# Kernel tuning notes

Hardware: AMD Instinct MI355X
Metric: run time of the kernel (lower is better)

Reference implementation:

```python
import jax, jax.numpy as jnp
import numpy as np

B, C_IN, IMG, P, G, E, H = 4, 3, 576, 16, 36, 768, 12
T = G * G  # 1296 tokens
HD = E // H  # 64
LN_EPS = 1e-5


def layer_norm(x, g, b):
    mu = jnp.mean(x, axis=-1, keepdims=True)
    var = jnp.mean((x - mu) ** 2, axis=-1, keepdims=True)
    return (x - mu) * jax.lax.rsqrt(var + LN_EPS) * g + b


def setup_inputs() -> dict:
    key = jax.random.key(0)
    ks = jax.random.split(key, 12)
    s = lambda *sh: 0.02
    return {
        "x": jax.random.normal(ks[0], (B, C_IN, IMG, IMG), jnp.float32),
        "conv_w": jax.random.normal(ks[1], (E, C_IN, P, P), jnp.float32) * 0.02,
        "conv_b": jnp.zeros((E,), jnp.float32),
        "wq": jax.random.normal(ks[2], (E, E), jnp.float32) * 0.02,
        "wk": jax.random.normal(ks[3], (E, E), jnp.float32) * 0.02,
        "wv": jax.random.normal(ks[4], (E, E), jnp.float32) * 0.02,
        "wo": jax.random.normal(ks[5], (E, E), jnp.float32) * 0.02,
        "bo": jnp.zeros((E,), jnp.float32),
        "w1": jax.random.normal(ks[6], (E, 4 * E), jnp.float32) * 0.02,
        "b1": jnp.zeros((4 * E,), jnp.float32),
        "w2": jax.random.normal(ks[7], (4 * E, E), jnp.float32) * 0.02,
        "b2": jnp.zeros((E,), jnp.float32),
        "ln1_g": jnp.ones((E,), jnp.float32),
        "ln1_b": jnp.zeros((E,), jnp.float32),
        "ln2_g": jnp.ones((E,), jnp.float32),
        "ln2_b": jnp.zeros((E,), jnp.float32),
    }


def reference(x, conv_w, conv_b, wq, wk, wv, wo, bo, w1, b1, w2, b2,
              ln1_g, ln1_b, ln2_g, ln2_b):
    # --- patch embed: stride==kernel conv as patch reshape + einsum ---
    xr = x.reshape(B, C_IN, G, P, G, P)  # b c i p j q
    tok = jnp.einsum('bcipjq,ecpq->bije', xr, conv_w) + conv_b
    tok = tok.reshape(B, T, E)  # row-major (i,j) matches flatten(2).transpose

    # --- causal multi-head attention (scale uses n_embd, as in source) ---
    h = layer_norm(tok, ln1_g, ln1_b)
    q = (h @ wq).reshape(B, T, H, HD)
    k = (h @ wk).reshape(B, T, H, HD)
    v = (h @ wv).reshape(B, T, H, HD)
    scores = jnp.einsum('bqhd,bkhd->bhqk', q, k) * (E ** -0.5)
    mask = jnp.tril(jnp.ones((T, T), bool))
    scores = jnp.where(mask, scores, -jnp.inf)
    attn = jax.nn.softmax(scores, axis=-1)
    ao = jnp.einsum('bhqk,bkhd->bqhd', attn, v).reshape(B, T, E)
    tok = tok + (ao @ wo + bo)

    # --- MLP ---
    h2 = layer_norm(tok, ln2_g, ln2_b)
    tok = tok + (jax.nn.relu(h2 @ w1 + b1) @ w2 + b2)

    # --- back to image grid ---
    return tok.reshape(B, G, G, E).transpose(0, 3, 1, 2)
```

## Files before the change

kernel.cpp:

```cpp
#include <hip/hip_runtime.h>

typedef unsigned short u16;
typedef unsigned int u32;
typedef unsigned long long u64;
typedef float f32x4 __attribute__((ext_vector_type(4)));
typedef __bf16 bf16x8 __attribute__((ext_vector_type(8)));
typedef u16 u16x8 __attribute__((ext_vector_type(8)));

#define DEV __device__ __forceinline__


DEV u16 f2bf(float f) {
    union { float f; u32 u; } un; un.f = f;
    u32 u = un.u;
    return (u16)((u + 0x7fffu + ((u >> 16) & 1u)) >> 16);
}

DEV void gll16(const u16* src, u16* dst) {
    auto g = (const __attribute__((address_space(1))) u32*)(src);
    auto s = (__attribute__((address_space(3))) u32*)(dst);
    __builtin_amdgcn_global_load_lds(g, s, 16, 0, 0);
}

__global__ void convcvt_k(const float* __restrict__ src, u16* __restrict__ dst) {
    int i = blockIdx.x * 256 + threadIdx.x;
    f32x4 v = ((const f32x4*)src)[i];
    union { u16 q[4]; u64 ll; } un;
    #pragma unroll
    for (int j = 0; j < 4; ++j) un.q[j] = f2bf(v[j]);
    ((u64*)dst)[i] = un.ll;
}

__global__ void wtrans_k(const float* __restrict__ src, u16* __restrict__ dst, int K, int N) {
    __shared__ float tile[32][33];
    int n0 = blockIdx.x * 32, k0 = blockIdx.y * 32;
    int tx = threadIdx.x & 31, ty = threadIdx.x >> 5;
    #pragma unroll
    for (int i = 0; i < 32; i += 8)
        tile[ty + i][tx] = src[(size_t)(k0 + ty + i) * N + n0 + tx];
    __syncthreads();
    #pragma unroll
    for (int i = 0; i < 32; i += 8)
        dst[(size_t)(n0 + ty + i) * K + k0 + tx] = f2bf(tile[tx][ty + i]);
}

__global__ void patch_k(const float* __restrict__ x, u16* __restrict__ out) {
    int idx = blockIdx.x * 256 + threadIdx.x;
    int j = idx % 36; int r1 = idx / 36;
    int p = r1 % 16;  int r2 = r1 / 16;
    int i = r2 % 36;  int r3 = r2 / 36;
    int c = r3 % 3;   int b = r3 / 3;
    const f32x4* src = (const f32x4*)(x + (size_t)((b * 3 + c) * 576 + i * 16 + p) * 576 + j * 16);
    u16x8 lo, hi;
    #pragma unroll
    for (int k = 0; k < 2; ++k) {
        f32x4 v = src[k];
        #pragma unroll
        for (int e = 0; e < 4; ++e) lo[k * 4 + e] = f2bf(v[e]);
    }
    #pragma unroll
    for (int k = 0; k < 2; ++k) {
        f32x4 v = src[2 + k];
        #pragma unroll
        for (int e = 0; e < 4; ++e) hi[k * 4 + e] = f2bf(v[e]);
    }
    u16* dst = out + (size_t)(b * 1296 + i * 36 + j) * 768 + c * 256 + p * 16;
    *(u16x8*)dst = lo;
    *(u16x8*)(dst + 8) = hi;
}

__global__ __launch_bounds__(256) void ln_k(const float* __restrict__ x, const float* __restrict__ g,
                                            const float* __restrict__ bta, u16* __restrict__ out) {
    int row = blockIdx.x * 4 + (threadIdx.x >> 6);
    int l = threadIdx.x & 63;
    const float* xr = x + (size_t)row * 768;
    float v[12]; float s = 0.f, s2 = 0.f;
    #pragma unroll
    for (int i = 0; i < 12; ++i) { v[i] = xr[l + 64 * i]; s += v[i]; s2 += v[i] * v[i]; }
    #pragma unroll
    for (int off = 32; off; off >>= 1) { s += __shfl_xor(s, off); s2 += __shfl_xor(s2, off); }
    float mu = s * (1.f / 768.f);
    float var = s2 * (1.f / 768.f) - mu * mu;
    float rs = rsqrtf(var + 1e-5f);
    u16* orow = out + (size_t)row * 768;
    #pragma unroll
    for (int i = 0; i < 12; ++i) {
        int c = l + 64 * i;
        orow[c] = f2bf((v[i] - mu) * rs * g[c] + bta[c]);
    }
}

__global__ void vtrans_k(const u16* __restrict__ qkv, u16* __restrict__ vt) {
    __shared__ u16 tile[32][33];
    int bh = blockIdx.z; int b = bh / 12, h = bh % 12;
    int t0 = blockIdx.x * 32, d0 = blockIdx.y * 32;
    int tx = threadIdx.x & 31, ty = threadIdx.x >> 5;
    #pragma unroll
    for (int i = 0; i < 32; i += 8) {
        int t = t0 + ty + i; int tc = min(t, 1295);
        tile[ty + i][tx] = qkv[(size_t)(b * 1296 + tc) * 2304 + 1536 + h * 64 + d0 + tx];
    }
    __syncthreads();
    #pragma unroll
    for (int i = 0; i < 32; i += 8) {
        int d = d0 + ty + i; int t = t0 + tx;
        if (t < 1296) vt[(size_t)(bh * 64 + d) * 1344 + t] = tile[tx][ty + i];
    }
}

template <int BN, int EPI>
__global__ __launch_bounds__(256) void gemm_k(const u16* __restrict__ A, const u16* __restrict__ Bt,
                                              const float* __restrict__ bias, const float* __restrict__ resid,
                                              void* __restrict__ Cout, int K, int ldc, int nbx) {
    constexpr int M = 5184;
    constexpr int NF = BN / 32;
    __shared__ __align__(16) u16 lds[2][(128 + BN) * 64];
    const int tid = threadIdx.x;
    const int l = tid & 63, w = tid >> 6;
    const int lr = l & 15, lq = l >> 4;
    const int wm = w >> 1, wn = w & 1;

    const int total = nbx * 41;
    const int q = total >> 3, r = total & 7;
    const int x = blockIdx.x & 7;
    const int j = blockIdx.x >> 3;
    const int wrk = x * q + min(x, r) + j;
    const int by = wrk / nbx, bx = wrk - by * nbx;
    const int bm = by * 128;
    const int bn = bx * BN;

    f32x4 acc[4][NF];
    f32x4 zz = {0.f, 0.f, 0.f, 0.f};
    #pragma unroll
    for (int i = 0; i < 4; ++i)
        #pragma unroll
        for (int jj = 0; jj < NF; ++jj) acc[i][jj] = zz;

    const int nk = K >> 6;

    auto stage = [&](int buf, int kt) {
        u16* abase = &lds[buf][0];
        #pragma unroll
        for (int i = 0; i < 4; ++i) {
            int slot = tid + i * 256;
            int row = slot >> 3, piece = slot & 7;
            int sp = piece ^ (row & 7);
            const u16* src = A + (size_t)min(bm + row, M - 1) * K + kt * 64 + sp * 8;
            gll16(src, abase + ((tid & ~63) + i * 256) * 8);
        }
        u16* bbase = &lds[buf][128 * 64];
        #pragma unroll
        for (int i = 0; i < NF; ++i) {
            int slot = tid + i * 256;
            int row = slot >> 3, piece = slot & 7;
            int sp = piece ^ (row & 7);
            const u16* src = Bt + (size_t)(bn + row) * K + kt * 64 + sp * 8;
            gll16(src, bbase + ((tid & ~63) + i * 256) * 8);
        }
    };

    stage(0, 0);
    __syncthreads();
    for (int kt = 0; kt < nk; ++kt) {
        int cur = kt & 1;
        if (kt + 1 < nk) stage(cur ^ 1, kt + 1);
        bf16x8 af[4][2], bfr[NF][2];
        #pragma unroll
        for (int mi = 0; mi < 4; ++mi) {
            int row = wm * 64 + mi * 16 + lr;
            #pragma unroll
            for (int ks = 0; ks < 2; ++ks)
                af[mi][ks] = *(const bf16x8*)&lds[cur][row * 64 + (((lq + 4 * ks) ^ (row & 7)) << 3)];
        }
        #pragma unroll
        for (int ni = 0; ni < NF; ++ni) {
            int row = wn * (BN / 2) + ni * 16 + lr;
            #pragma unroll
            for (int ks = 0; ks < 2; ++ks)
                bfr[ni][ks] = *(const bf16x8*)&lds[cur][128 * 64 + row * 64 + (((lq + 4 * ks) ^ (row & 7)) << 3)];
        }
        #pragma unroll
        for (int mi = 0; mi < 4; ++mi)
            #pragma unroll
            for (int ni = 0; ni < NF; ++ni) {
                acc[mi][ni] = __builtin_amdgcn_mfma_f32_16x16x32_bf16(af[mi][0], bfr[ni][0], acc[mi][ni], 0, 0, 0);
                acc[mi][ni] = __builtin_amdgcn_mfma_f32_16x16x32_bf16(af[mi][1], bfr[ni][1], acc[mi][ni], 0, 0, 0);
            }
        __syncthreads();
    }

    #pragma unroll
    for (int mi = 0; mi < 4; ++mi) {
        #pragma unroll
        for (int ni = 0; ni < NF; ++ni) {
            int col = bn + wn * (BN / 2) + ni * 16 + lr;
            float bv = 0.f;
            if constexpr (EPI != 1) bv = bias[col];
            #pragma unroll
            for (int rr = 0; rr < 4; ++rr) {
                int m = bm + wm * 64 + mi * 16 + 4 * lq + rr;
                if (m < M) {
                    float v = acc[mi][ni][rr] + bv;
                    if constexpr (EPI == 2) v = fmaxf(v, 0.f);
                    if constexpr (EPI == 3 || EPI == 4) v += resid[(size_t)m * ldc + col];
                    if constexpr (EPI == 0 || EPI == 3) {
                        ((float*)Cout)[(size_t)m * ldc + col] = v;
                    } else if constexpr (EPI == 4) {
                        int b = m / 1296, t = m - b * 1296;
                        ((float*)Cout)[(size_t)(b * 768 + col) * 1296 + t] = v;
                    } else {
                        ((u16*)Cout)[(size_t)m * ldc + col] = f2bf(v);
                    }
                }
            }
        }
    }
}

__global__ __launch_bounds__(256, 2) void attn_k(const u16* __restrict__ qkv, const u16* __restrict__ vt,
                                                 u16* __restrict__ ao) {
    const float SCALE = 0.03608439182435161f;
    __shared__ __align__(16) u16 kv[2][2][4096];
    __shared__ __align__(16) u16 plds[4][16 * 72];
    const int tid = threadIdx.x;
    const int wid = tid >> 6, l = tid & 63;
    const int id = blockIdx.x;
    const int xr = id & 7, sl = id >> 3;
    const int g = sl / 11, bx = sl - g * 11;
    const int bh = g * 8 + xr;
    const int b = bh / 12, h = bh % 12;
    const int uu = bx * 4 + wid;
    const int u = min(uu, 40);
    const bool valid = (uu <= 40);
    const int lr = l & 15, lq = l >> 4;
    const int q0S = 16 * u, q0L = 16 * (80 - u);
    const bool hasS = valid && (u < 40);
    const int nktS = (u < 40) ? (((q0S + 15) >> 6) + 1) : 0;
    const int nktL = ((q0L + 15) >> 6) + 1;
    const int umin = min(bx * 4, 40);
    const int nktmax = ((16 * (80 - umin) + 15) >> 6) + 1;

    const u16* kbase = qkv + (size_t)(b * 1296) * 2304 + 768 + h * 64;
    const u16* vbase = vt + (size_t)bh * 64 * 1344;
    u16* pl = &plds[wid][0];

    const u16* qpS = qkv + (size_t)(b * 1296 + q0S + lr) * 2304 + h * 64;
    const u16* qpL = qkv + (size_t)(b * 1296 + q0L + lr) * 2304 + h * 64;
    bf16x8 qS0 = *(const bf16x8*)(qpS + 8 * lq);
    bf16x8 qS1 = *(const bf16x8*)(qpS + 32 + 8 * lq);
    bf16x8 qL0 = *(const bf16x8*)(qpL + 8 * lq);
    bf16x8 qL1 = *(const bf16x8*)(qpL + 32 + 8 * lq);

    f32x4 zz = {0.f, 0.f, 0.f, 0.f};
    f32x4 oS[4], oL[4];
    float mS[4], mL[4], lSs[4], lLs[4];
    #pragma unroll
    for (int i = 0; i < 4; ++i) {
        oS[i] = zz; oL[i] = zz;
        mS[i] = -__builtin_inff(); mL[i] = -__builtin_inff();
        lSs[i] = 0.f; lLs[i] = 0.f;
    }

    auto stage = [&](int buf, int kt) {
        const int k0 = kt * 64;
        #pragma unroll
        for (int i = 0; i < 2; ++i) {
            int slot = tid + i * 256;
            int row = slot >> 3;
            int piece = slot & 7;
            int sp = piece ^ (row & 7);
            int tc = min(k0 + row, 1295);
            gll16(kbase + (size_t)tc * 2304 + sp * 8,
                  &kv[buf][0][((tid & 0xFFFFFFC0) + i * 256) * 8]);
        }
        #pragma unroll
        for (int i = 0; i < 2; ++i) {
            int slot = tid + i * 256;
            int row = slot >> 3;
            int piece = slot & 7;
            int sp = piece ^ (row & 7);
            gll16(vbase + (size_t)row * 1344 + k0 + sp * 8,
                  &kv[buf][1][((tid & 0xFFFFFFC0) + i * 256) * 8]);
        }
    };

    bf16x8 kb[4][2], vb[4][2];

    auto visit = [&](int q0, bf16x8 qa0, bf16x8 qa1, f32x4 (&o)[4],
                     float (&mrow)[4], float (&lsum)[4], int k0) {
        f32x4 s[4];
        #pragma unroll
        for (int nt = 0; nt < 4; ++nt) {
            f32x4 a = zz;
            a = __builtin_amdgcn_mfma_f32_16x16x32_bf16(qa0, kb[nt][0], a, 0, 0, 0);
            a = __builtin_amdgcn_mfma_f32_16x16x32_bf16(qa1, kb[nt][1], a, 0, 0, 0);
            s[nt] = a;
        }
        float tmax[4];
        #pragma unroll
        for (int r = 0; r < 4; ++r) {
            int qrow = q0 + 4 * lq + r;
            #pragma unroll
            for (int nt = 0; nt < 4; ++nt) {
                int tcol = k0 + nt * 16 + lr;
                float val = s[nt][r] * SCALE;
                s[nt][r] = (tcol <= qrow) ? val : -__builtin_inff();
            }
            tmax[r] = fmaxf(fmaxf(s[0][r], s[1][r]), fmaxf(s[2][r], s[3][r]));
        }
        #pragma unroll
        for (int off = 1; off < 16; off <<= 1)
            #pragma unroll
            for (int r = 0; r < 4; ++r) tmax[r] = fmaxf(tmax[r], __shfl_xor(tmax[r], off));
        float alpha[4], tsum[4];
        #pragma unroll
        for (int r = 0; r < 4; ++r) {
            float nm = fmaxf(mrow[r], tmax[r]);
            alpha[r] = __expf(mrow[r] - nm);
            mrow[r] = nm;
            float accp = 0.f;
            #pragma unroll
            for (int nt = 0; nt < 4; ++nt) {
                float p = __expf(s[nt][r] - nm);
                s[nt][r] = p;
                accp += p;
            }
            tsum[r] = accp;
        }
        #pragma unroll
        for (int off = 1; off < 16; off <<= 1)
            #pragma unroll
            for (int r = 0; r < 4; ++r) tsum[r] += __shfl_xor(tsum[r], off);
        #pragma unroll
        for (int r = 0; r < 4; ++r) lsum[r] = lsum[r] * alpha[r] + tsum[r];
        #pragma unroll
        for (int dt = 0; dt < 4; ++dt)
            #pragma unroll
            for (int r = 0; r < 4; ++r) o[dt][r] *= alpha[r];
        #pragma unroll
        for (int nt = 0; nt < 4; ++nt)
            #pragma unroll
            for (int r = 0; r < 4; ++r)
                pl[(4 * lq + r) * 72 + nt * 16 + lr] = f2bf(s[nt][r]);
        __builtin_amdgcn_wave_barrier();
        bf16x8 pa0 = *(const bf16x8*)&pl[lr * 72 + 8 * lq];
        bf16x8 pa1 = *(const bf16x8*)&pl[lr * 72 + 32 + 8 * lq];
        #pragma unroll
        for (int dt = 0; dt < 4; ++dt) {
            o[dt] = __builtin_amdgcn_mfma_f32_16x16x32_bf16(pa0, vb[dt][0], o[dt], 0, 0, 0);
            o[dt] = __builtin_amdgcn_mfma_f32_16x16x32_bf16(pa1, vb[dt][1], o[dt], 0, 0, 0);
        }
        __builtin_amdgcn_wave_barrier();
    };

    stage(0, 0);
    for (int kt = 0; kt < nktmax; ++kt) {
        const int cur = kt & 1;
        const int k0 = kt * 64;
        __syncthreads();
        if (kt + 1 < nktmax) stage(cur ^ 1, kt + 1);
        #pragma unroll
        for (int nt = 0; nt < 4; ++nt) {
            int krow = nt * 16 + lr;
            kb[nt][0] = *(const bf16x8*)&kv[cur][0][krow * 64 + ((lq ^ (krow & 7)) << 3)];
            kb[nt][1] = *(const bf16x8*)&kv[cur][0][krow * 64 + (((lq + 4) ^ (krow & 7)) << 3)];
        }
        #pragma unroll
        for (int dt = 0; dt < 4; ++dt) {
            int vrow = dt * 16 + lr;
            vb[dt][0] = *(const bf16x8*)&kv[cur][1][vrow * 64 + ((lq ^ (vrow & 7)) << 3)];
            vb[dt][1] = *(const bf16x8*)&kv[cur][1][vrow * 64 + (((lq + 4) ^ (vrow & 7)) << 3)];
        }
        if (valid && kt < nktS) visit(q0S, qS0, qS1, oS, mS, lSs, k0);
        if (valid && kt < nktL) visit(q0L, qL0, qL1, oL, mL, lLs, k0);
    }

    if (valid) {
        #pragma unroll
        for (int dt = 0; dt < 4; ++dt)
            #pragma unroll
            for (int r = 0; r < 4; ++r) {
                if (hasS) {
                    int qrow = q0S + 4 * lq + r;
                    ao[(size_t)(b * 1296 + qrow) * 768 + h * 64 + dt * 16 + lr] = f2bf(oS[dt][r] / lSs[r]);
                }
                int qrowL = q0L + 4 * lq + r;
                ao[(size_t)(b * 1296 + qrowL) * 768 + h * 64 + dt * 16 + lr] = f2bf(oL[dt][r] / lLs[r]);
            }
    }
}

extern "C" void kernel_launch(void* const* d_in, const int* in_sizes, int n_in,
                              void* d_out, int out_size, void* d_ws, size_t ws_size,
                              hipStream_t stream) {
    const float* x      = (const float*)d_in[0];
    const float* conv_w = (const float*)d_in[1];
    const float* conv_b = (const float*)d_in[2];
    const float* wq     = (const float*)d_in[3];
    const float* wk     = (const float*)d_in[4];
    const float* wv     = (const float*)d_in[5];
    const float* wo     = (const float*)d_in[6];
    const float* bo     = (const float*)d_in[7];
    const float* w1     = (const float*)d_in[8];
    const float* b1     = (const float*)d_in[9];
    const float* w2     = (const float*)d_in[10];
    const float* b2     = (const float*)d_in[11];
    const float* ln1g   = (const float*)d_in[12];
    const float* ln1b   = (const float*)d_in[13];
    const float* ln2g   = (const float*)d_in[14];
    const float* ln2b   = (const float*)d_in[15];

    char* ws = (char*)d_ws;
    size_t off = 0;
    auto alloc = [&](size_t bytes) { char* p = ws + off; off = (off + bytes + 255) & ~(size_t)255; return p; };
    u16*   convw_bf = (u16*)alloc((size_t)768 * 768 * 2);
    u16*   wqkv_t   = (u16*)alloc((size_t)2304 * 768 * 2);
    u16*   wo_t     = (u16*)alloc((size_t)768 * 768 * 2);
    u16*   w1_t     = (u16*)alloc((size_t)3072 * 768 * 2);
    u16*   w2_t     = (u16*)alloc((size_t)768 * 3072 * 2);
    float* tok      = (float*)alloc((size_t)5184 * 768 * 4);
    u16*   hbuf     = (u16*)alloc((size_t)5184 * 768 * 2);
    u16*   apao     = (u16*)alloc((size_t)5184 * 768 * 2);
    size_t qkv_bytes = ((size_t)5184 * 2304 * 2 + 255) & ~(size_t)255;
    size_t vt_bytes  = (size_t)48 * 64 * 1344 * 2;
    size_t a1_bytes  = (size_t)5184 * 3072 * 2;
    size_t big_bytes = qkv_bytes + vt_bytes;
    if (a1_bytes > big_bytes) big_bytes = a1_bytes;
    char* big = alloc(big_bytes);
    u16* qkvb = (u16*)big;
    u16* vtb  = (u16*)(big + qkv_bytes);
    u16* a1   = (u16*)big;

    convcvt_k<<<576, 256, 0, stream>>>(conv_w, convw_bf);
    wtrans_k<<<dim3(24, 24), 256, 0, stream>>>(wq, wqkv_t, 768, 768);
    wtrans_k<<<dim3(24, 24), 256, 0, stream>>>(wk, wqkv_t + 768 * 768, 768, 768);
    wtrans_k<<<dim3(24, 24), 256, 0, stream>>>(wv, wqkv_t + 2 * 768 * 768, 768, 768);
    wtrans_k<<<dim3(24, 24), 256, 0, stream>>>(wo, wo_t, 768, 768);
    wtrans_k<<<dim3(96, 24), 256, 0, stream>>>(w1, w1_t, 768, 3072);
    wtrans_k<<<dim3(24, 96), 256, 0, stream>>>(w2, w2_t, 3072, 768);
    patch_k<<<972, 256, 0, stream>>>(x, apao);
    gemm_k<64, 0><<<12 * 41, 256, 0, stream>>>(apao, convw_bf, conv_b, nullptr, tok, 768, 768, 12);
    ln_k<<<1296, 256, 0, stream>>>(tok, ln1g, ln1b, hbuf);
    gemm_k<128, 1><<<18 * 41, 256, 0, stream>>>(hbuf, wqkv_t, nullptr, nullptr, qkvb, 768, 2304, 18);
    vtrans_k<<<dim3(41, 2, 48), 256, 0, stream>>>(qkvb, vtb);
    attn_k<<<528, 256, 0, stream>>>(qkvb, vtb, apao);
    gemm_k<64, 3><<<12 * 41, 256, 0, stream>>>(apao, wo_t, bo, tok, tok, 768, 768, 12);
    ln_k<<<1296, 256, 0, stream>>>(tok, ln2g, ln2b, hbuf);
    gemm_k<128, 2><<<24 * 41, 256, 0, stream>>>(hbuf, w1_t, b1, nullptr, a1, 768, 3072, 24);
    gemm_k<64, 4><<<12 * 41, 256, 0, stream>>>(a1, w2_t, b2, tok, d_out, 3072, 768, 12);
}
```

Baseline: 350.8 us.

## Transpose attention MFMA operands so each lane owns one query row

Swaps the A/B operands of the QK^T and PV MFMAs so each lane holds a single query row's scores across four keys. Row max and row sum then need only two cross-lane shuffles instead of four shuffle rounds per register. The scale is folded into one fma before the exp, P is written to LDS and the output to global memory as packed bf16x4 vectors, and s_setprio is raised around the MFMA blocks. The cost is a different rounding path through __builtin_convertvector and a reliance on the transposed layout being correct.

```diff
diff --git a/kernel.cpp b/kernel.cpp
--- a/kernel.cpp
+++ b/kernel.cpp
@@ -5,6 +5,7 @@
 typedef unsigned long long u64;
 typedef float f32x4 __attribute__((ext_vector_type(4)));
 typedef __bf16 bf16x8 __attribute__((ext_vector_type(8)));
+typedef __bf16 bf16x4 __attribute__((ext_vector_type(4)));
 typedef u16 u16x8 __attribute__((ext_vector_type(8)));
 
 #define DEV __device__ __forceinline__
@@ -252,14 +253,11 @@
     bf16x8 qL1 = *(const bf16x8*)(qpL + 32 + 8 * lq);
 
     f32x4 zz = {0.f, 0.f, 0.f, 0.f};
+    const float NEG = -__builtin_inff();
     f32x4 oS[4], oL[4];
-    float mS[4], mL[4], lSs[4], lLs[4];
-    #pragma unroll
-    for (int i = 0; i < 4; ++i) {
-        oS[i] = zz; oL[i] = zz;
-        mS[i] = -__builtin_inff(); mL[i] = -__builtin_inff();
-        lSs[i] = 0.f; lLs[i] = 0.f;
-    }
+    float mS = NEG, mL = NEG, lS = 0.f, lL = 0.f;
+    #pragma unroll
+    for (int i = 0; i < 4; ++i) { oS[i] = zz; oL[i] = zz; }
 
     auto stage = [&](int buf, int kt) {
         const int k0 = kt * 64;
@@ -287,69 +285,66 @@
     bf16x8 kb[4][2], vb[4][2];
 
     auto visit = [&](int q0, bf16x8 qa0, bf16x8 qa1, f32x4 (&o)[4],
-                     float (&mrow)[4], float (&lsum)[4], int k0) {
+                     float& mrow, float& lsum, int k0) {
+        const int qrow = q0 + lr;
         f32x4 s[4];
+        __builtin_amdgcn_s_setprio(1);
         #pragma unroll
         for (int nt = 0; nt < 4; ++nt) {
             f32x4 a = zz;
-            a = __builtin_amdgcn_mfma_f32_16x16x32_bf16(qa0, kb[nt][0], a, 0, 0, 0);
-            a = __builtin_amdgcn_mfma_f32_16x16x32_bf16(qa1, kb[nt][1], a, 0, 0, 0);
+            a = __builtin_amdgcn_mfma_f32_16x16x32_bf16(kb[nt][0], qa0, a, 0, 0, 0);
+            a = __builtin_amdgcn_mfma_f32_16x16x32_bf16(kb[nt][1], qa1, a, 0, 0, 0);
             s[nt] = a;
         }
-        float tmax[4];
-        #pragma unroll
-        for (int r = 0; r < 4; ++r) {
-            int qrow = q0 + 4 * lq + r;
-            #pragma unroll
-            for (int nt = 0; nt < 4; ++nt) {
-                int tcol = k0 + nt * 16 + lr;
-                float val = s[nt][r] * SCALE;
-                s[nt][r] = (tcol <= qrow) ? val : -__builtin_inff();
+        __builtin_amdgcn_s_setprio(0);
+        float mnt[4];
+        #pragma unroll
+        for (int nt = 0; nt < 4; ++nt) {
+            #pragma unroll
+            for (int r = 0; r < 4; ++r) {
+                int k = k0 + nt * 16 + 4 * lq + r;
+                s[nt][r] = (k <= qrow) ? s[nt][r] : NEG;
             }
-            tmax[r] = fmaxf(fmaxf(s[0][r], s[1][r]), fmaxf(s[2][r], s[3][r]));
-        }
-        #pragma unroll
-        for (int off = 1; off < 16; off <<= 1)
-            #pragma unroll
-            for (int r = 0; r < 4; ++r) tmax[r] = fmaxf(tmax[r], __shfl_xor(tmax[r], off));
-        float alpha[4], tsum[4];
-        #pragma unroll
-        for (int r = 0; r < 4; ++r) {
-            float nm = fmaxf(mrow[r], tmax[r]);
-            alpha[r] = __expf(mrow[r] - nm);
-            mrow[r] = nm;
-            float accp = 0.f;
-            #pragma unroll
-            for (int nt = 0; nt < 4; ++nt) {
-                float p = __expf(s[nt][r] - nm);
+            mnt[nt] = fmaxf(fmaxf(s[nt][0], s[nt][1]), fmaxf(s[nt][2], s[nt][3]));
+        }
+        float mx = fmaxf(fmaxf(mnt[0], mnt[1]), fmaxf(mnt[2], mnt[3]));
+        mx = fmaxf(mx, __shfl_xor(mx, 16));
+        mx = fmaxf(mx, __shfl_xor(mx, 32));
+        float nm = fmaxf(mrow, mx);
+        float alpha = __expf(SCALE * (mrow - nm));
+        mrow = nm;
+        float nbase = -SCALE * nm;
+        float tnt[4];
+        #pragma unroll
+        for (int nt = 0; nt < 4; ++nt) {
+            #pragma unroll
+            for (int r = 0; r < 4; ++r) {
+                float p = __expf(fmaf(s[nt][r], SCALE, nbase));
                 s[nt][r] = p;
-                accp += p;
             }
-            tsum[r] = accp;
-        }
-        #pragma unroll
-        for (int off = 1; off < 16; off <<= 1)
-            #pragma unroll
-            for (int r = 0; r < 4; ++r) tsum[r] += __shfl_xor(tsum[r], off);
-        #pragma unroll
-        for (int r = 0; r < 4; ++r) lsum[r] = lsum[r] * alpha[r] + tsum[r];
-        #pragma unroll
-        for (int dt = 0; dt < 4; ++dt)
-            #pragma unroll
-            for (int r = 0; r < 4; ++r) o[dt][r] *= alpha[r];
-        #pragma unroll
-        for (int nt = 0; nt < 4; ++nt)
-            #pragma unroll
-            for (int r = 0; r < 4; ++r)
-                pl[(4 * lq + r) * 72 + nt * 16 + lr] = f2bf(s[nt][r]);
+            tnt[nt] = (s[nt][0] + s[nt][1]) + (s[nt][2] + s[nt][3]);
+        }
+        float ts = (tnt[0] + tnt[1]) + (tnt[2] + tnt[3]);
+        ts += __shfl_xor(ts, 16);
+        ts += __shfl_xor(ts, 32);
+        lsum = lsum * alpha + ts;
+        #pragma unroll
+        for (int dt = 0; dt < 4; ++dt) o[dt] *= alpha;
+        #pragma unroll
+        for (int nt = 0; nt < 4; ++nt) {
+            bf16x4 pv = __builtin_convertvector(s[nt], bf16x4);
+            *(bf16x4*)&pl[lr * 72 + nt * 16 + 4 * lq] = pv;
+        }
         __builtin_amdgcn_wave_barrier();
         bf16x8 pa0 = *(const bf16x8*)&pl[lr * 72 + 8 * lq];
         bf16x8 pa1 = *(const bf16x8*)&pl[lr * 72 + 32 + 8 * lq];
+        __builtin_amdgcn_s_setprio(1);
         #pragma unroll
         for (int dt = 0; dt < 4; ++dt) {
-            o[dt] = __builtin_amdgcn_mfma_f32_16x16x32_bf16(pa0, vb[dt][0], o[dt], 0, 0, 0);
-            o[dt] = __builtin_amdgcn_mfma_f32_16x16x32_bf16(pa1, vb[dt][1], o[dt], 0, 0, 0);
-        }
+            o[dt] = __builtin_amdgcn_mfma_f32_16x16x32_bf16(vb[dt][0], pa0, o[dt], 0, 0, 0);
+            o[dt] = __builtin_amdgcn_mfma_f32_16x16x32_bf16(vb[dt][1], pa1, o[dt], 0, 0, 0);
+        }
+        __builtin_amdgcn_s_setprio(0);
         __builtin_amdgcn_wave_barrier();
     };
 
@@ -371,22 +366,27 @@
             vb[dt][0] = *(const bf16x8*)&kv[cur][1][vrow * 64 + ((lq ^ (vrow & 7)) << 3)];
             vb[dt][1] = *(const bf16x8*)&kv[cur][1][vrow * 64 + (((lq + 4) ^ (vrow & 7)) << 3)];
         }
-        if (valid && kt < nktS) visit(q0S, qS0, qS1, oS, mS, lSs, k0);
-        if (valid && kt < nktL) visit(q0L, qL0, qL1, oL, mL, lLs, k0);
+        if (valid && kt < nktS) visit(q0S, qS0, qS1, oS, mS, lS, k0);
+        if (valid && kt < nktL) visit(q0L, qL0, qL1, oL, mL, lL, k0);
     }
 
     if (valid) {
-        #pragma unroll
-        for (int dt = 0; dt < 4; ++dt)
-            #pragma unroll
-            for (int r = 0; r < 4; ++r) {
-                if (hasS) {
-                    int qrow = q0S + 4 * lq + r;
-                    ao[(size_t)(b * 1296 + qrow) * 768 + h * 64 + dt * 16 + lr] = f2bf(oS[dt][r] / lSs[r]);
-                }
-                int qrowL = q0L + 4 * lq + r;
-                ao[(size_t)(b * 1296 + qrowL) * 768 + h * 64 + dt * 16 + lr] = f2bf(oL[dt][r] / lLs[r]);
+        if (hasS) {
+            float inv = 1.f / lS;
+            u16* aoS = ao + (size_t)(b * 1296 + q0S + lr) * 768 + h * 64 + 4 * lq;
+            #pragma unroll
+            for (int dt = 0; dt < 4; ++dt) {
+                f32x4 ov = oS[dt] * inv;
+                *(bf16x4*)(aoS + dt * 16) = __builtin_convertvector(ov, bf16x4);
             }
+        }
+        float invL = 1.f / lL;
+        u16* aoL = ao + (size_t)(b * 1296 + q0L + lr) * 768 + h * 64 + 4 * lq;
+        #pragma unroll
+        for (int dt = 0; dt < 4; ++dt) {
+            f32x4 ov = oL[dt] * invL;
+            *(bf16x4*)(aoL + dt * 16) = __builtin_convertvector(ov, bf16x4);
+        }
     }
 }
 
```

Result: faster. 338.3 us (-3.6%).
